# Kernel tuning notes

Hardware: AMD Instinct MI355X
Metric: run time of the kernel (lower is better)

The kernel has to match this reference:

```python
import jax, jax.numpy as jnp
import numpy as np
from jax import lax

B, T, V, E, H = 64, 20, 32000, 256, 512
EPS = 1e-5


def _conv_bn_relu(x, w, b, g, beta, m, v):
    # x: (B,C,H,W), w: (O,I,3,3), stride 2, pad 1; BN in eval mode with running stats
    y = lax.conv_general_dilated(x, w, (2, 2), ((1, 1), (1, 1)),
                                 dimension_numbers=('NCHW', 'OIHW', 'NCHW'))
    y = y + b[None, :, None, None]
    inv = g / jnp.sqrt(v + EPS)
    y = y * inv[None, :, None, None] + (beta - m * inv)[None, :, None, None]
    return jax.nn.relu(y)


def setup_inputs() -> dict:
    key = jax.random.key(0)
    ks = iter(jax.random.split(key, 40))
    s = 0.05
    d = {}
    d['images'] = jax.random.normal(next(ks), (B, 3, 64, 64), jnp.float32)
    d['captions'] = jax.random.randint(next(ks), (B, T), 0, V)
    chans = [3, 64, 128, 256, 512]
    for i in range(4):
        ci, co = chans[i], chans[i + 1]
        d[f'conv{i+1}_w'] = jax.random.normal(next(ks), (co, ci, 3, 3), jnp.float32) * s
        d[f'conv{i+1}_b'] = jnp.zeros((co,), jnp.float32)
        d[f'bn{i+1}_g'] = jnp.ones((co,), jnp.float32)
        d[f'bn{i+1}_b'] = jnp.zeros((co,), jnp.float32)
        d[f'bn{i+1}_m'] = jnp.zeros((co,), jnp.float32)
        d[f'bn{i+1}_v'] = jnp.ones((co,), jnp.float32)
    d['proj_w'] = jax.random.normal(next(ks), (E, 512), jnp.float32) * s
    d['proj_b'] = jnp.zeros((E,), jnp.float32)
    d['emb'] = jax.random.normal(next(ks), (V, E), jnp.float32) * s
    d['att_wv'] = jax.random.normal(next(ks), (H, E), jnp.float32) * s
    d['att_bv'] = jnp.zeros((H,), jnp.float32)
    d['att_wt'] = jax.random.normal(next(ks), (H, H), jnp.float32) * s
    d['att_bt'] = jnp.zeros((H,), jnp.float32)
    d['att_wa'] = jax.random.normal(next(ks), (1, H), jnp.float32) * s
    d['att_ba'] = jnp.zeros((1,), jnp.float32)
    d['w_ih'] = jax.random.normal(next(ks), (4 * H, 2 * E), jnp.float32) * s
    d['w_hh'] = jax.random.normal(next(ks), (4 * H, H), jnp.float32) * s
    d['b_ih'] = jnp.zeros((4 * H,), jnp.float32)
    d['b_hh'] = jnp.zeros((4 * H,), jnp.float32)
    d['out_w'] = jax.random.normal(next(ks), (V, H), jnp.float32) * s
    d['out_b'] = jnp.zeros((V,), jnp.float32)
    return d


def reference(images, captions,
              conv1_w, conv1_b, bn1_g, bn1_b, bn1_m, bn1_v,
              conv2_w, conv2_b, bn2_g, bn2_b, bn2_m, bn2_v,
              conv3_w, conv3_b, bn3_g, bn3_b, bn3_m, bn3_v,
              conv4_w, conv4_b, bn4_g, bn4_b, bn4_m, bn4_v,
              proj_w, proj_b, emb,
              att_wv, att_bv, att_wt, att_bt, att_wa, att_ba,
              w_ih, w_hh, b_ih, b_hh, out_w, out_b):
    # --- image encoder ---
    x = _conv_bn_relu(images, conv1_w, conv1_b, bn1_g, bn1_b, bn1_m, bn1_v)
    x = _conv_bn_relu(x, conv2_w, conv2_b, bn2_g, bn2_b, bn2_m, bn2_v)
    x = _conv_bn_relu(x, conv3_w, conv3_b, bn3_g, bn3_b, bn3_m, bn3_v)
    x = _conv_bn_relu(x, conv4_w, conv4_b, bn4_g, bn4_b, bn4_m, bn4_v)  # (B,512,4,4)
    b, c, h_, w_ = x.shape
    visual = x.reshape(b, c, h_ * w_).transpose(0, 2, 1)  # (B,R=16,512)
    visual = visual @ proj_w.T + proj_b                    # (B,R,E)

    v_proj = visual @ att_wv.T + att_bv                    # (B,R,H) - precompute

    emb_seq = emb[captions].transpose(1, 0, 2)             # (T,B,E)

    def step(carry, word_embed):
        h, cst = carry
        # attention over regions conditioned on previous h
        t = h @ att_wt.T + att_bt                          # (B,H)
        comb = jnp.tanh(v_proj + t[:, None, :])            # (B,R,H)
        scores = jnp.einsum('brh,h->br', comb, att_wa[0]) + att_ba[0]
        attw = jax.nn.softmax(scores, axis=1)              # (B,R)
        attended = jnp.einsum('br,bre->be', attw, visual)  # (B,E)
        xin = jnp.concatenate([word_embed, attended], axis=1)  # (B,2E)
        gates = xin @ w_ih.T + b_ih + h @ w_hh.T + b_hh    # (B,4H)
        i, f, g, o = jnp.split(gates, 4, axis=1)           # torch gate order i,f,g,o
        cst = jax.nn.sigmoid(f) * cst + jax.nn.sigmoid(i) * jnp.tanh(g)
        h = jax.nn.sigmoid(o) * jnp.tanh(cst)
        logits = h @ out_w.T + out_b                       # (B,V)
        return (h, cst), logits

    h0 = jnp.zeros((b, H), visual.dtype)
    c0 = jnp.zeros((b, H), visual.dtype)
    _, logits = lax.scan(step, (h0, c0), emb_seq)          # (T,B,V)
    return logits.transpose(1, 0, 2)                       # (B,T,V)
```

## Files before the change

kernel.cpp:

```cpp
#include <hip/hip_runtime.h>
#include <hip/hip_bf16.h>
#include <cstdint>
#include <cstddef>

typedef __attribute__((ext_vector_type(8))) short short8;
typedef __attribute__((ext_vector_type(4))) float floatx4;

__device__ inline float bf2f(unsigned short u) {
  union { unsigned int i; float f; } v; v.i = ((unsigned int)u) << 16; return v.f;
}
__device__ inline unsigned short f2bf(float f) {
  union { float f; unsigned int i; } v; v.f = f;
  unsigned int u = v.i;
  return (unsigned short)((u + 0x7FFFu + ((u >> 16) & 1u)) >> 16);
}
__device__ inline short8 ld8(const unsigned short* p) {
  return *reinterpret_cast<const short8*>(p);
}
__device__ inline float sigmoidf_(float x) { return 1.0f / (1.0f + __expf(-x)); }
__device__ inline float tanh_fast(float x) {
  float e = __expf(2.0f * x);
  return 1.0f - 2.0f / (e + 1.0f);
}

#define AT_LD(p)    __hip_atomic_load((p), __ATOMIC_RELAXED, __HIP_MEMORY_SCOPE_AGENT)
#define AT_ST(p, v) __hip_atomic_store((p), (v), __ATOMIC_RELAXED, __HIP_MEMORY_SCOPE_AGENT)
#define WAITCNT0()  asm volatile("s_waitcnt vmcnt(0) lgkmcnt(0)" ::: "memory")
#define CFENCE()    asm volatile("" ::: "memory")

static const size_t OFF_WIH   = 0;
static const size_t OFF_WHH   = 2097152;
static const size_t OFF_VPROJ = 4194304;
static const size_t OFF_VISE  = 5242880;
static const size_t OFF_HS    = 5767168;
static const size_t OFF_XIN   = 7077888;
static const size_t OFF_H0    = 7143424;
static const size_t OFF_H1    = 7208960;
static const size_t OFF_CT    = 7274496;
static const size_t OFF_W1PAD = 7405568;
static const size_t OFF_CW2   = 7409664;
static const size_t OFF_CW3   = 7557120;
static const size_t OFF_CW4   = 8146944;
static const size_t OFF_PRJW  = 10506240;
static const size_t OFF_ATWV  = 10768384;
static const size_t OFF_ACT1  = 11030528;
static const size_t OFF_ACT3  = 11030528;
static const size_t OFF_ACT2  = 19419136;
static const size_t OFF_ACT4  = 19419136;
static const size_t OFF_VISA  = 20467712;
static const size_t OFF_COL   = 23613440;
static const size_t OFF_BAR   = 28332032;
static const size_t OFF_ATWT  = 28348416;
static const size_t OFF_BIG   = 28872704;
static const size_t NEED_BIG  = OFF_BIG + 32768000;

__global__ void cvt_k(const float* __restrict__ s, unsigned short* __restrict__ d, int n4)
{
  int i = blockIdx.x * 256 + threadIdx.x;
  if (i < n4) {
    float4 v = reinterpret_cast<const float4*>(s)[i];
    ushort4 o;
    o.x = f2bf(v.x); o.y = f2bf(v.y); o.z = f2bf(v.z); o.w = f2bf(v.w);
    reinterpret_cast<ushort4*>(d)[i] = o;
  }
}

struct CvtArgs {
  const float* s[8];
  unsigned short* d[8];
  int cum[9];
};
__global__ void cvtall_k(CvtArgs a)
{
  int i = blockIdx.x * 256 + threadIdx.x;
  if (i >= a.cum[8]) return;
  int seg = 0;
  while (seg < 7 && i >= a.cum[seg + 1]) ++seg;
  int j = i - a.cum[seg];
  float4 v = reinterpret_cast<const float4*>(a.s[seg])[j];
  ushort4 o;
  o.x = f2bf(v.x); o.y = f2bf(v.y); o.z = f2bf(v.z); o.w = f2bf(v.w);
  reinterpret_cast<ushort4*>(a.d[seg])[j] = o;
}

__global__ void init_k(const float* __restrict__ conv1_w, unsigned short* __restrict__ w1pad,
                       unsigned short* __restrict__ h0, unsigned int* __restrict__ bar)
{
  int i = blockIdx.x * 256 + threadIdx.x;
  if (i < 64 * 32) {
    int co = i >> 5, k = i & 31;
    w1pad[i] = (k < 27) ? f2bf(conv1_w[co * 27 + k]) : (unsigned short)0;
  }
  if (i < 64 * 512) h0[i] = 0;
  if (i < 4096) bar[i] = 0u;
}

__global__ void im2col1_k(const float* __restrict__ in, unsigned short* __restrict__ col)
{
  int o = blockIdx.x * 256 + threadIdx.x;
  int n = o >> 5, k = o & 31;
  unsigned short v = 0;
  if (k < 27) {
    int b = n >> 10, y = (n >> 5) & 31, x = n & 31;
    int ci = k / 9, r9 = k - ci * 9, ky = r9 / 3, kx = r9 - ky * 3;
    int iy = 2 * y - 1 + ky, ix = 2 * x - 1 + kx;
    if (iy >= 0 && iy < 64 && ix >= 0 && ix < 64)
      v = f2bf(in[(((size_t)b * 3 + ci) << 12) + (iy << 6) + ix]);
  }
  col[o] = v;
}

__global__ void im2col_k(const unsigned short* __restrict__ in, unsigned short* __restrict__ col,
                         int Cin, int Hin, int Win, int Kreal, int Kpad, int lgHW, int lgW,
                         int n0)
{
  const int ng = n0 + blockIdx.x;
  const int b = ng >> lgHW;
  const int yx = ng & ((1 << lgHW) - 1);
  const int y = yx >> lgW;
  const int x = yx & ((1 << lgW) - 1);
  const int iy0 = 2 * y - 1;
  const int ix0 = 2 * x - 1;
  for (int k = threadIdx.x; k < Kpad; k += blockDim.x) {
    unsigned short v = 0;
    if (k < Kreal) {
      int ci = k / 9;
      int r9 = k - ci * 9;
      int ky = r9 / 3;
      int kx = r9 - ky * 3;
      int iy = iy0 + ky, ix = ix0 + kx;
      if (iy >= 0 && iy < Hin && ix >= 0 && ix < Win) {
        size_t idx = (((size_t)b * Cin + ci) * Hin + iy) * Win + ix;
        v = in[idx];
      }
    }
    col[(size_t)blockIdx.x * Kpad + k] = v;
  }
}

__global__ void visa_k(const unsigned short* __restrict__ act4, unsigned short* __restrict__ visA)
{
  int o = blockIdx.x * 256 + threadIdx.x;
  int c = o & 511, br = o >> 9;
  int b = br >> 4, r = br & 15;
  visA[o] = act4[(((size_t)b * 512 + c) << 4) + r];
}

template<int EPI>
__global__ __launch_bounds__(256)
void gemm_k(const unsigned short* __restrict__ A, const unsigned short* __restrict__ B,
            int K, int N, void* __restrict__ outp,
            const float* __restrict__ cb, const float* __restrict__ bg,
            const float* __restrict__ bb, const float* __restrict__ bm,
            const float* __restrict__ bv, int Cout, int lgHW,
            const float* __restrict__ biasN, int n_base, int ldOut)
{
  const int w   = threadIdx.x >> 6;
  const int l   = threadIdx.x & 63;
  const int l15 = l & 15;
  const int q   = l >> 4;
  const int m0  = blockIdx.y * 64;
  const int n0  = blockIdx.x * 256 + w * 64;
  const unsigned short* Ap = A + (size_t)(m0 + l15) * K + q * 8;
  const unsigned short* Bp = B + (size_t)(n0 + l15) * K + q * 8;

  floatx4 acc[4][4];
  #pragma unroll
  for (int i = 0; i < 4; i++)
    #pragma unroll
    for (int j = 0; j < 4; j++)
      acc[i][j] = (floatx4){0.f, 0.f, 0.f, 0.f};

  for (int kc = 0; kc < K; kc += 32) {
    short8 a0 = ld8(Ap + kc);
    short8 a1 = ld8(Ap + (size_t)16 * K + kc);
    short8 a2 = ld8(Ap + (size_t)32 * K + kc);
    short8 a3 = ld8(Ap + (size_t)48 * K + kc);
    #pragma unroll
    for (int nf = 0; nf < 4; nf++) {
      short8 bf = ld8(Bp + (size_t)(nf * 16) * K + kc);
      acc[0][nf] = __builtin_amdgcn_mfma_f32_16x16x32_bf16(a0, bf, acc[0][nf], 0, 0, 0);
      acc[1][nf] = __builtin_amdgcn_mfma_f32_16x16x32_bf16(a1, bf, acc[1][nf], 0, 0, 0);
      acc[2][nf] = __builtin_amdgcn_mfma_f32_16x16x32_bf16(a2, bf, acc[2][nf], 0, 0, 0);
      acc[3][nf] = __builtin_amdgcn_mfma_f32_16x16x32_bf16(a3, bf, acc[3][nf], 0, 0, 0);
    }
  }
  #pragma unroll
  for (int mf = 0; mf < 4; mf++) {
    #pragma unroll
    for (int r = 0; r < 4; r++) {
      int m = m0 + mf * 16 + q * 4 + r;
      float scale = 1.0f, shift = 0.0f;
      if (EPI == 0) {
        float inv = bg[m] / sqrtf(bv[m] + 1e-5f);
        scale = inv;
        shift = (cb[m] - bm[m]) * inv + bb[m];
      }
      #pragma unroll
      for (int nf = 0; nf < 4; nf++) {
        int n = n0 + nf * 16 + l15;
        float c = acc[mf][nf][r];
        if (EPI == 0) {
          c = fmaxf(c * scale + shift, 0.0f);
          int ng = n_base + n;
          int bi = ng >> lgHW;
          int yx = ng & ((1 << lgHW) - 1);
          ((unsigned short*)outp)[(((size_t)bi * Cout + m) << lgHW) + yx] = f2bf(c);
        } else if (EPI == 1) {
          ((unsigned short*)outp)[(size_t)m * N + n] = f2bf(c + biasN[n]);
        } else {
          ((float*)outp)[(size_t)m * ldOut + n_base + n] = c + biasN[n_base + n];
        }
      }
    }
  }
}

__global__ __launch_bounds__(256)
void rec_k(const unsigned short* __restrict__ w_ih, const unsigned short* __restrict__ w_hh,
           const float* __restrict__ b_ih, const float* __restrict__ b_hh,
           const unsigned short* __restrict__ vproj, const unsigned short* __restrict__ visE,
           const unsigned short* __restrict__ atwt, const float* __restrict__ att_bt,
           const float* __restrict__ att_wa, const float* __restrict__ att_ba,
           const int* __restrict__ captions, const float* __restrict__ emb,
           unsigned int* xin_u, unsigned int* h0_u, unsigned int* h1_u,
           unsigned short* __restrict__ hs, unsigned int* __restrict__ bar)
{
  __shared__ __align__(16) float sH[512];
  __shared__ float sT[512];
  __shared__ float sA[256];
  __shared__ float sSc[16];
  __shared__ float sAw[16];
  __shared__ __align__(16) unsigned short sB[64 * 256];
  __shared__ float sG[4][16][64];

  unsigned int* xf = bar;
  unsigned int* hf = bar + 64;

  const int tid = threadIdx.x;
  const int bid = blockIdx.x;
  const int w   = tid >> 6;
  const int l   = tid & 63;
  const int l15 = l & 15;
  const int q   = l >> 4;
  const int u0  = bid * 16;
  const int arow = w * 512 + u0 + l15;
  const unsigned short* wihRow = w_ih + (size_t)arow * 512;
  const unsigned short* whhRow = w_hh + (size_t)arow * 512;

  float creg[4];
  float bsum[4][4];
  if (bid < 32) {
    const int batch = tid & 63;
    const int g0 = tid >> 6;
    (void)batch;
    #pragma unroll
    for (int s = 0; s < 4; ++s) {
      creg[s] = 0.0f;
      int u = u0 + g0 * 4 + s;
      #pragma unroll
      for (int g = 0; g < 4; ++g)
        bsum[s][g] = b_ih[g * 512 + u] + b_hh[g * 512 + u];
    }
  }

  #define STAGE_TILE(SRC_EXPR)                                              \
    {                                                                       \
      _Pragma("unroll")                                                     \
      for (int i_ = 0; i_ < 16; ++i_) {                                     \
        int p_ = i_ * 256 + tid;                                            \
        int row_ = p_ >> 6, cu_ = p_ & 63;                                  \
        unsigned long long v_ = (SRC_EXPR);                                 \
        reinterpret_cast<unsigned long long*>(sB)[(row_ * 64 + cu_) ^ ((row_ & 7) << 1)] = v_; \
      }                                                                     \
    }

  #define MFMA_SEG(APTR)                                                    \
    {                                                                       \
      const unsigned short* Ap_ = (APTR);                                   \
      _Pragma("unroll")                                                     \
      for (int kc = 0; kc < 256; kc += 32) {                                \
        short8 a_ = ld8(Ap_ + kc);                                          \
        _Pragma("unroll")                                                   \
        for (int nt = 0; nt < 4; ++nt) {                                    \
          int row_ = l15 + nt * 16;                                         \
          short8 bf_ = *reinterpret_cast<const short8*>(                    \
              sB + ((row_ * 256 + q * 8 + kc) ^ ((row_ & 7) << 3)));        \
          acc[nt] = __builtin_amdgcn_mfma_f32_16x16x32_bf16(a_, bf_, acc[nt], 0, 0, 0); \
        }                                                                   \
      }                                                                     \
    }

  for (int t = 0; t < 20; ++t) {
    unsigned int* hin_u  = (t & 1) ? h1_u : h0_u;
    unsigned int* hout_u = (t & 1) ? h0_u : h1_u;

    if (t > 0) {
      if (tid < 32) {
        while ((int)AT_LD(hf + tid) < t) __builtin_amdgcn_s_sleep(1);
      }
      __syncthreads();
      CFENCE();
    }

    {
      const int b = bid;
      unsigned int hv = AT_LD(hin_u + b * 256 + tid);
      sH[2 * tid]     = bf2f((unsigned short)(hv & 0xffffu));
      sH[2 * tid + 1] = bf2f((unsigned short)(hv >> 16));
      __syncthreads();

      {
        const unsigned short* w0 = atwt + (size_t)tid * 512;
        const unsigned short* w1 = w0 + (size_t)256 * 512;
        float a0 = 0.f, a1 = 0.f;
        #pragma unroll 2
        for (int k = 0; k < 512; k += 8) {
          short8 x0 = ld8(w0 + k);
          short8 x1 = ld8(w1 + k);
          #pragma unroll
          for (int j = 0; j < 8; ++j) {
            float hk = sH[k + j];
            a0 += bf2f((unsigned short)x0[j]) * hk;
            a1 += bf2f((unsigned short)x1[j]) * hk;
          }
        }
        sT[tid]       = a0 + att_bt[tid];
        sT[tid + 256] = a1 + att_bt[tid + 256];
      }
      __syncthreads();

      {
        int r = tid >> 4, l16 = tid & 15;
        const unsigned short* vp = vproj + ((size_t)b * 16 + r) * 512;
        float s = 0.0f;
        #pragma unroll 4
        for (int i = 0; i < 32; ++i) {
          int k = i * 16 + l16;
          s += tanh_fast(bf2f(vp[k]) + sT[k]) * att_wa[k];
        }
        for (int d = 8; d >= 1; d >>= 1) s += __shfl_down(s, d, 16);
        if (l16 == 0) sSc[r] = s + att_ba[0];
      }
      __syncthreads();

      if (tid < 16) {
        float s = sSc[tid];
        float m = s;
        for (int d = 8; d >= 1; d >>= 1) m = fmaxf(m, __shfl_xor(m, d, 16));
        float e = __expf(s - m);
        float sum = e;
        for (int d = 8; d >= 1; d >>= 1) sum += __shfl_xor(sum, d, 16);
        sAw[tid] = e / sum;
      }
      __syncthreads();

      {
        float a = 0.0f;
        #pragma unroll
        for (int r = 0; r < 16; r++)
          a += sAw[r] * bf2f(visE[((size_t)b * 16 + r) * 256 + tid]);
        sA[tid] = a;
      }
      __syncthreads();

      if (tid < 128) {
        AT_ST(xin_u + b * 128 + tid,
              (unsigned int)f2bf(sA[2 * tid]) | ((unsigned int)f2bf(sA[2 * tid + 1]) << 16));
      }
      WAITCNT0();
      __syncthreads();
      if (tid == 0) AT_ST(xf + bid, (unsigned int)(t + 1));
    }

    if (bid < 32) {
      floatx4 acc[4];
      #pragma unroll
      for (int nt = 0; nt < 4; nt++) acc[nt] = (floatx4){0.f, 0.f, 0.f, 0.f};

      {
        #pragma unroll
        for (int i_ = 0; i_ < 16; ++i_) {
          int p_ = i_ * 256 + tid;
          int row_ = p_ >> 6, c4_ = p_ & 63;
          int cap_ = captions[row_ * 20 + t];
          float4 ev = *reinterpret_cast<const float4*>(emb + (size_t)cap_ * 256 + c4_ * 4);
          unsigned long long v_ =
              (unsigned long long)f2bf(ev.x) |
              ((unsigned long long)f2bf(ev.y) << 16) |
              ((unsigned long long)f2bf(ev.z) << 32) |
              ((unsigned long long)f2bf(ev.w) << 48);
          reinterpret_cast<unsigned long long*>(sB)[(row_ * 64 + c4_) ^ ((row_ & 7) << 1)] = v_;
        }
      }
      __syncthreads();
      MFMA_SEG(wihRow + q * 8);
      __syncthreads();

      const unsigned long long* hull = reinterpret_cast<const unsigned long long*>(hin_u);
      STAGE_TILE(AT_LD(hull + ((i_ * 256 + tid) >> 6) * 128 + ((i_ * 256 + tid) & 63)));
      __syncthreads();
      MFMA_SEG(whhRow + q * 8);
      __syncthreads();
      STAGE_TILE(AT_LD(hull + ((i_ * 256 + tid) >> 6) * 128 + 64 + ((i_ * 256 + tid) & 63)));
      __syncthreads();
      MFMA_SEG(whhRow + 256 + q * 8);
      __syncthreads();

      if (tid < 64) {
        while ((int)AT_LD(xf + tid) < t + 1) __builtin_amdgcn_s_sleep(1);
      }
      __syncthreads();
      CFENCE();

      const unsigned long long* xull = reinterpret_cast<const unsigned long long*>(xin_u);
      STAGE_TILE(AT_LD(xull + ((i_ * 256 + tid) >> 6) * 64 + ((i_ * 256 + tid) & 63)));
      __syncthreads();
      MFMA_SEG(wihRow + 256 + q * 8);
      __syncthreads();

      #pragma unroll
      for (int nt = 0; nt < 4; nt++)
        #pragma unroll
        for (int r = 0; r < 4; r++)
          sG[w][q * 4 + r][nt * 16 + l15] = acc[nt][r];
      __syncthreads();

      const int batch = tid & 63;
      const int g0 = tid >> 6;
      #pragma unroll
      for (int s = 0; s < 4; s += 2) {
        float hn2[2];
        #pragma unroll
        for (int d = 0; d < 2; ++d) {
          int um = g0 * 4 + s + d;
          float ii = sG[0][um][batch] + bsum[s + d][0];
          float ff = sG[1][um][batch] + bsum[s + d][1];
          float gg = sG[2][um][batch] + bsum[s + d][2];
          float oo = sG[3][um][batch] + bsum[s + d][3];
          float cn = sigmoidf_(ff) * creg[s + d] + sigmoidf_(ii) * tanh_fast(gg);
          hn2[d] = sigmoidf_(oo) * tanh_fast(cn);
          creg[s + d] = cn;
        }
        int u = u0 + g0 * 4 + s;
        unsigned int hp = (unsigned int)f2bf(hn2[0]) | ((unsigned int)f2bf(hn2[1]) << 16);
        AT_ST(hout_u + batch * 256 + (u >> 1), hp);
        *reinterpret_cast<unsigned int*>(hs + ((size_t)batch * 20 + t) * 512 + u) = hp;
      }
      WAITCNT0();
      __syncthreads();
      if (tid == 0) AT_ST(hf + bid, (unsigned int)(t + 1));
    }
  }
  #undef STAGE_TILE
  #undef MFMA_SEG
}

extern "C" void kernel_launch(void* const* d_in, const int* in_sizes, int n_in,
                              void* d_out, int out_size, void* d_ws, size_t ws_size,
                              hipStream_t stream)
{
  const float* images   = (const float*)d_in[0];
  const int*   captions = (const int*)d_in[1];
  const float* cw[4] = {(const float*)d_in[2],  (const float*)d_in[8],
                        (const float*)d_in[14], (const float*)d_in[20]};
  const float* cbp[4] = {(const float*)d_in[3],  (const float*)d_in[9],
                         (const float*)d_in[15], (const float*)d_in[21]};
  const float* bgp[4] = {(const float*)d_in[4],  (const float*)d_in[10],
                         (const float*)d_in[16], (const float*)d_in[22]};
  const float* bbp[4] = {(const float*)d_in[5],  (const float*)d_in[11],
                         (const float*)d_in[17], (const float*)d_in[23]};
  const float* bmp[4] = {(const float*)d_in[6],  (const float*)d_in[12],
                         (const float*)d_in[18], (const float*)d_in[24]};
  const float* bvp[4] = {(const float*)d_in[7],  (const float*)d_in[13],
                         (const float*)d_in[19], (const float*)d_in[25]};
  const float* proj_w = (const float*)d_in[26];
  const float* proj_b = (const float*)d_in[27];
  const float* emb    = (const float*)d_in[28];
  const float* att_wv = (const float*)d_in[29];
  const float* att_bv = (const float*)d_in[30];
  const float* att_wt = (const float*)d_in[31];
  const float* att_bt = (const float*)d_in[32];
  const float* att_wa = (const float*)d_in[33];
  const float* att_ba = (const float*)d_in[34];
  const float* w_ih   = (const float*)d_in[35];
  const float* w_hh   = (const float*)d_in[36];
  const float* b_ih   = (const float*)d_in[37];
  const float* b_hh   = (const float*)d_in[38];
  const float* out_w  = (const float*)d_in[39];
  const float* out_b  = (const float*)d_in[40];

  char* W = (char*)d_ws;
  unsigned short* wih_b = (unsigned short*)(W + OFF_WIH);
  unsigned short* whh_b = (unsigned short*)(W + OFF_WHH);
  unsigned short* vproj = (unsigned short*)(W + OFF_VPROJ);
  unsigned short* visE  = (unsigned short*)(W + OFF_VISE);
  unsigned short* hs    = (unsigned short*)(W + OFF_HS);
  unsigned short* xin   = (unsigned short*)(W + OFF_XIN);
  unsigned short* h0    = (unsigned short*)(W + OFF_H0);
  unsigned short* h1    = (unsigned short*)(W + OFF_H1);
  unsigned short* w1pad = (unsigned short*)(W + OFF_W1PAD);
  unsigned short* cw2_b = (unsigned short*)(W + OFF_CW2);
  unsigned short* cw3_b = (unsigned short*)(W + OFF_CW3);
  unsigned short* cw4_b = (unsigned short*)(W + OFF_CW4);
  unsigned short* prw_b = (unsigned short*)(W + OFF_PRJW);
  unsigned short* awv_b = (unsigned short*)(W + OFF_ATWV);
  unsigned short* atwt_b= (unsigned short*)(W + OFF_ATWT);
  unsigned short* act1  = (unsigned short*)(W + OFF_ACT1);
  unsigned short* act2  = (unsigned short*)(W + OFF_ACT2);
  unsigned short* act3  = (unsigned short*)(W + OFF_ACT3);
  unsigned short* act4  = (unsigned short*)(W + OFF_ACT4);
  unsigned short* visA  = (unsigned short*)(W + OFF_VISA);
  unsigned short* col   = (unsigned short*)(W + OFF_COL);
  unsigned int*   bar   = (unsigned int*)(W + OFF_BAR);
  const bool big = (ws_size >= NEED_BIG);
  unsigned short* colb  = big ? (unsigned short*)(W + OFF_BIG) : col;

  init_k<<<128, 256, 0, stream>>>(cw[0], w1pad, h0, bar);

  {
    CvtArgs ca;
    ca.s[0] = w_ih;   ca.d[0] = wih_b;
    ca.s[1] = w_hh;   ca.d[1] = whh_b;
    ca.s[2] = cw[1];  ca.d[2] = cw2_b;
    ca.s[3] = cw[2];  ca.d[3] = cw3_b;
    ca.s[4] = cw[3];  ca.d[4] = cw4_b;
    ca.s[5] = proj_w; ca.d[5] = prw_b;
    ca.s[6] = att_wv; ca.d[6] = awv_b;
    ca.s[7] = att_wt; ca.d[7] = atwt_b;
    int c0 = 0;
    int cnt[8] = {262144, 262144, 18432, 73728, 294912, 32768, 32768, 65536};
    ca.cum[0] = 0;
    for (int i = 0; i < 8; i++) { c0 += cnt[i]; ca.cum[i + 1] = c0; }
    cvtall_k<<<(c0 + 255) / 256, 256, 0, stream>>>(ca);
  }

  im2col1_k<<<8192, 256, 0, stream>>>(images, col);
  gemm_k<0><<<dim3(256, 1), 256, 0, stream>>>(w1pad, col, 32, 65536, act1,
      cbp[0], bgp[0], bbp[0], bmp[0], bvp[0], 64, 10, nullptr, 0, 0);

  if (big) {
    im2col_k<<<16384, 256, 0, stream>>>(act1, colb, 64, 32, 32, 576, 576, 8, 4, 0);
    gemm_k<0><<<dim3(64, 2), 256, 0, stream>>>(cw2_b, colb, 576, 16384, act2,
        cbp[1], bgp[1], bbp[1], bmp[1], bvp[1], 128, 8, nullptr, 0, 0);
    im2col_k<<<4096, 256, 0, stream>>>(act2, colb, 128, 16, 16, 1152, 1152, 6, 3, 0);
    gemm_k<0><<<dim3(16, 4), 256, 0, stream>>>(cw3_b, colb, 1152, 4096, act3,
        cbp[2], bgp[2], bbp[2], bmp[2], bvp[2], 256, 6, nullptr, 0, 0);
  } else {
    for (int c = 0; c < 4; c++) {
      im2col_k<<<4096, 256, 0, stream>>>(act1, col, 64, 32, 32, 576, 576, 8, 4, c * 4096);
      gemm_k<0><<<dim3(16, 2), 256, 0, stream>>>(cw2_b, col, 576, 4096, act2,
          cbp[1], bgp[1], bbp[1], bmp[1], bvp[1], 128, 8, nullptr, c * 4096, 0);
    }
    for (int c = 0; c < 2; c++) {
      im2col_k<<<2048, 256, 0, stream>>>(act2, col, 128, 16, 16, 1152, 1152, 6, 3, c * 2048);
      gemm_k<0><<<dim3(8, 4), 256, 0, stream>>>(cw3_b, col, 1152, 2048, act3,
          cbp[2], bgp[2], bbp[2], bmp[2], bvp[2], 256, 6, nullptr, c * 2048, 0);
    }
  }
  im2col_k<<<1024, 256, 0, stream>>>(act3, col, 256, 8, 8, 2304, 2304, 4, 2, 0);
  gemm_k<0><<<dim3(4, 8), 256, 0, stream>>>(cw4_b, col, 2304, 1024, act4,
      cbp[3], bgp[3], bbp[3], bmp[3], bvp[3], 512, 4, nullptr, 0, 0);

  visa_k<<<2048, 256, 0, stream>>>(act4, visA);
  gemm_k<1><<<dim3(1, 16), 256, 0, stream>>>(visA, prw_b, 512, 256, visE,
      nullptr, nullptr, nullptr, nullptr, nullptr, 0, 0, proj_b, 0, 0);
  gemm_k<1><<<dim3(2, 16), 256, 0, stream>>>(visE, awv_b, 256, 512, vproj,
      nullptr, nullptr, nullptr, nullptr, nullptr, 0, 0, att_bv, 0, 0);

  rec_k<<<64, 256, 0, stream>>>(wih_b, whh_b, b_ih, b_hh, vproj, visE,
                                atwt_b, att_bt, att_wa, att_ba, captions, emb,
                                (unsigned int*)xin, (unsigned int*)h0, (unsigned int*)h1,
                                hs, bar);

  if (big) {
    unsigned short* owb = (unsigned short*)(W + OFF_BIG);
    cvt_k<<<16000, 256, 0, stream>>>(out_w, owb, 32000 * 512 / 4);
    gemm_k<2><<<dim3(125, 20), 256, 0, stream>>>(hs, owb, 512, 32000,
        d_out, nullptr, nullptr, nullptr, nullptr, nullptr, 0, 0, out_b, 0, 32000);
  } else {
    for (int c = 0; c < 8; c++) {
      int rows = (c < 7) ? 4096 : 3328;
      const float* src = out_w + (size_t)c * 4096 * 512;
      cvt_k<<<rows / 2, 256, 0, stream>>>(src, col, rows * 512 / 4);
      gemm_k<2><<<dim3(rows / 256, 20), 256, 0, stream>>>(hs, col, 512, rows,
          d_out, nullptr, nullptr, nullptr, nullptr, nullptr, 0, 0, out_b, c * 4096, 32000);
    }
  }
}
```

Before: 1.687 ms.

## Use per-timestep buffers and flags in recurrent kernel, skip t=0 h work

The recurrent kernel now writes x and h into separate per-timestep buffers and signals completion with per-timestep boolean flags, replacing double-buffered h and monotonic counters. Reads of those buffers become plain loads instead of atomic loads. The t=0 attention matvec and W_hh MFMA are skipped because h0 is zero, and flag clearing moves into visa_k, so init_k no longer zeroes h0. This reduces per-step synchronization and load overhead in a latency-bound loop, at the cost of more workspace and a reliance on plain loads seeing data published before the flag.

Measured after the change: 1.551 ms. 1.09x faster.

```diff
diff --git a/kernel.cpp b/kernel.cpp
--- a/kernel.cpp
+++ b/kernel.cpp
@@ -33,10 +33,6 @@
 static const size_t OFF_VPROJ = 4194304;
 static const size_t OFF_VISE  = 5242880;
 static const size_t OFF_HS    = 5767168;
-static const size_t OFF_XIN   = 7077888;
-static const size_t OFF_H0    = 7143424;
-static const size_t OFF_H1    = 7208960;
-static const size_t OFF_CT    = 7274496;
 static const size_t OFF_W1PAD = 7405568;
 static const size_t OFF_CW2   = 7409664;
 static const size_t OFF_CW3   = 7557120;
@@ -48,8 +44,10 @@
 static const size_t OFF_ACT2  = 19419136;
 static const size_t OFF_ACT4  = 19419136;
 static const size_t OFF_VISA  = 20467712;
+static const size_t OFF_XB    = 21516288;
+static const size_t OFF_HB    = 22171648;
+static const size_t OFF_FLG   = 23482368;
 static const size_t OFF_COL   = 23613440;
-static const size_t OFF_BAR   = 28332032;
 static const size_t OFF_ATWT  = 28348416;
 static const size_t OFF_BIG   = 28872704;
 static const size_t NEED_BIG  = OFF_BIG + 32768000;
@@ -83,16 +81,13 @@
   reinterpret_cast<ushort4*>(a.d[seg])[j] = o;
 }
 
-__global__ void init_k(const float* __restrict__ conv1_w, unsigned short* __restrict__ w1pad,
-                       unsigned short* __restrict__ h0, unsigned int* __restrict__ bar)
+__global__ void init_k(const float* __restrict__ conv1_w, unsigned short* __restrict__ w1pad)
 {
   int i = blockIdx.x * 256 + threadIdx.x;
   if (i < 64 * 32) {
     int co = i >> 5, k = i & 31;
     w1pad[i] = (k < 27) ? f2bf(conv1_w[co * 27 + k]) : (unsigned short)0;
   }
-  if (i < 64 * 512) h0[i] = 0;
-  if (i < 4096) bar[i] = 0u;
 }
 
 __global__ void im2col1_k(const float* __restrict__ in, unsigned short* __restrict__ col)
@@ -138,12 +133,14 @@
   }
 }
 
-__global__ void visa_k(const unsigned short* __restrict__ act4, unsigned short* __restrict__ visA)
+__global__ void visa_k(const unsigned short* __restrict__ act4, unsigned short* __restrict__ visA,
+                       unsigned int* __restrict__ flg)
 {
   int o = blockIdx.x * 256 + threadIdx.x;
   int c = o & 511, br = o >> 9;
   int b = br >> 4, r = br & 15;
   visA[o] = act4[(((size_t)b * 512 + c) << 4) + r];
+  if (o < 2560) AT_ST(flg + o, 0u);
 }
 
 template<int EPI>
@@ -223,8 +220,8 @@
            const unsigned short* __restrict__ atwt, const float* __restrict__ att_bt,
            const float* __restrict__ att_wa, const float* __restrict__ att_ba,
            const int* __restrict__ captions, const float* __restrict__ emb,
-           unsigned int* xin_u, unsigned int* h0_u, unsigned int* h1_u,
-           unsigned short* __restrict__ hs, unsigned int* __restrict__ bar)
+           unsigned int* xb, unsigned int* hb, unsigned int* flg,
+           unsigned short* __restrict__ hs)
 {
   __shared__ __align__(16) float sH[512];
   __shared__ float sT[512];
@@ -233,9 +230,6 @@
   __shared__ float sAw[16];
   __shared__ __align__(16) unsigned short sB[64 * 256];
   __shared__ float sG[4][16][64];
-
-  unsigned int* xf = bar;
-  unsigned int* hf = bar + 64;
 
   const int tid = threadIdx.x;
   const int bid = blockIdx.x;
@@ -251,9 +245,7 @@
   float creg[4];
   float bsum[4][4];
   if (bid < 32) {
-    const int batch = tid & 63;
     const int g0 = tid >> 6;
-    (void)batch;
     #pragma unroll
     for (int s = 0; s < 4; ++s) {
       creg[s] = 0.0f;
@@ -292,12 +284,15 @@
     }
 
   for (int t = 0; t < 20; ++t) {
-    unsigned int* hin_u  = (t & 1) ? h1_u : h0_u;
-    unsigned int* hout_u = (t & 1) ? h0_u : h1_u;
+    const unsigned int* hbin = hb + (size_t)(t - 1) * 16384;
+    unsigned int* hbout = hb + (size_t)t * 16384;
+    unsigned int* xbt   = xb + (size_t)t * 8192;
+    unsigned int* flgt  = flg + (size_t)t * 128;
 
     if (t > 0) {
       if (tid < 32) {
-        while ((int)AT_LD(hf + tid) < t) __builtin_amdgcn_s_sleep(1);
+        while (AT_LD(flg + (size_t)(t - 1) * 128 + 64 + tid) == 0u)
+          __builtin_amdgcn_s_sleep(1);
       }
       __syncthreads();
       CFENCE();
@@ -305,12 +300,12 @@
 
     {
       const int b = bid;
-      unsigned int hv = AT_LD(hin_u + b * 256 + tid);
-      sH[2 * tid]     = bf2f((unsigned short)(hv & 0xffffu));
-      sH[2 * tid + 1] = bf2f((unsigned short)(hv >> 16));
-      __syncthreads();
-
-      {
+      if (t > 0) {
+        unsigned int hv = hbin[b * 256 + tid];
+        sH[2 * tid]     = bf2f((unsigned short)(hv & 0xffffu));
+        sH[2 * tid + 1] = bf2f((unsigned short)(hv >> 16));
+        __syncthreads();
+
         const unsigned short* w0 = atwt + (size_t)tid * 512;
         const unsigned short* w1 = w0 + (size_t)256 * 512;
         float a0 = 0.f, a1 = 0.f;
@@ -327,6 +322,9 @@
         }
         sT[tid]       = a0 + att_bt[tid];
         sT[tid + 256] = a1 + att_bt[tid + 256];
+      } else {
+        sT[tid]       = att_bt[tid];
+        sT[tid + 256] = att_bt[tid + 256];
       }
       __syncthreads();
 
@@ -364,13 +362,18 @@
       }
       __syncthreads();
 
-      if (tid < 128) {
-        AT_ST(xin_u + b * 128 + tid,
-              (unsigned int)f2bf(sA[2 * tid]) | ((unsigned int)f2bf(sA[2 * tid + 1]) << 16));
+      if (tid < 64) {
+        int j = 4 * tid;
+        unsigned long long v =
+            (unsigned long long)f2bf(sA[j]) |
+            ((unsigned long long)f2bf(sA[j + 1]) << 16) |
+            ((unsigned long long)f2bf(sA[j + 2]) << 32) |
+            ((unsigned long long)f2bf(sA[j + 3]) << 48);
+        AT_ST(reinterpret_cast<unsigned long long*>(xbt) + b * 64 + tid, v);
       }
       WAITCNT0();
       __syncthreads();
-      if (tid == 0) AT_ST(xf + bid, (unsigned int)(t + 1));
+      if (tid == 0) AT_ST(flgt + bid, 1u);
     }
 
     if (bid < 32) {
@@ -397,24 +400,26 @@
       MFMA_SEG(wihRow + q * 8);
       __syncthreads();
 
-      const unsigned long long* hull = reinterpret_cast<const unsigned long long*>(hin_u);
-      STAGE_TILE(AT_LD(hull + ((i_ * 256 + tid) >> 6) * 128 + ((i_ * 256 + tid) & 63)));
-      __syncthreads();
-      MFMA_SEG(whhRow + q * 8);
-      __syncthreads();
-      STAGE_TILE(AT_LD(hull + ((i_ * 256 + tid) >> 6) * 128 + 64 + ((i_ * 256 + tid) & 63)));
-      __syncthreads();
-      MFMA_SEG(whhRow + 256 + q * 8);
-      __syncthreads();
+      if (t > 0) {
+        const unsigned long long* hull = reinterpret_cast<const unsigned long long*>(hbin);
+        STAGE_TILE(hull[((i_ * 256 + tid) >> 6) * 128 + ((i_ * 256 + tid) & 63)]);
+        __syncthreads();
+        MFMA_SEG(whhRow + q * 8);
+        __syncthreads();
+        STAGE_TILE(hull[((i_ * 256 + tid) >> 6) * 128 + 64 + ((i_ * 256 + tid) & 63)]);
+        __syncthreads();
+        MFMA_SEG(whhRow + 256 + q * 8);
+        __syncthreads();
+      }
 
       if (tid < 64) {
-        while ((int)AT_LD(xf + tid) < t + 1) __builtin_amdgcn_s_sleep(1);
+        while (AT_LD(flgt + tid) == 0u) __builtin_amdgcn_s_sleep(1);
       }
       __syncthreads();
       CFENCE();
 
-      const unsigned long long* xull = reinterpret_cast<const unsigned long long*>(xin_u);
-      STAGE_TILE(AT_LD(xull + ((i_ * 256 + tid) >> 6) * 64 + ((i_ * 256 + tid) & 63)));
+      const unsigned long long* xull = reinterpret_cast<const unsigned long long*>(xbt);
+      STAGE_TILE(xull[((i_ * 256 + tid) >> 6) * 64 + ((i_ * 256 + tid) & 63)]);
       __syncthreads();
       MFMA_SEG(wihRow + 256 + q * 8);
       __syncthreads();
@@ -444,12 +449,12 @@
         }
         int u = u0 + g0 * 4 + s;
         unsigned int hp = (unsigned int)f2bf(hn2[0]) | ((unsigned int)f2bf(hn2[1]) << 16);
-        AT_ST(hout_u + batch * 256 + (u >> 1), hp);
+        AT_ST(hbout + batch * 256 + (u >> 1), hp);
         *reinterpret_cast<unsigned int*>(hs + ((size_t)batch * 20 + t) * 512 + u) = hp;
       }
       WAITCNT0();
       __syncthreads();
-      if (tid == 0) AT_ST(hf + bid, (unsigned int)(t + 1));
+      if (tid == 0) AT_ST(flgt + 64 + bid, 1u);
     }
   }
   #undef STAGE_TILE
@@ -496,9 +501,6 @@
   unsigned short* vproj = (unsigned short*)(W + OFF_VPROJ);
   unsigned short* visE  = (unsigned short*)(W + OFF_VISE);
   unsigned short* hs    = (unsigned short*)(W + OFF_HS);
-  unsigned short* xin   = (unsigned short*)(W + OFF_XIN);
-  unsigned short* h0    = (unsigned short*)(W + OFF_H0);
-  unsigned short* h1    = (unsigned short*)(W + OFF_H1);
   unsigned short* w1pad = (unsigned short*)(W + OFF_W1PAD);
   unsigned short* cw2_b = (unsigned short*)(W + OFF_CW2);
   unsigned short* cw3_b = (unsigned short*)(W + OFF_CW3);
@@ -512,11 +514,13 @@
   unsigned short* act4  = (unsigned short*)(W + OFF_ACT4);
   unsigned short* visA  = (unsigned short*)(W + OFF_VISA);
   unsigned short* col   = (unsigned short*)(W + OFF_COL);
-  unsigned int*   bar   = (unsigned int*)(W + OFF_BAR);
+  unsigned int*   xbp   = (unsigned int*)(W + OFF_XB);
+  unsigned int*   hbp   = (unsigned int*)(W + OFF_HB);
+  unsigned int*   flg   = (unsigned int*)(W + OFF_FLG);
   const bool big = (ws_size >= NEED_BIG);
   unsigned short* colb  = big ? (unsigned short*)(W + OFF_BIG) : col;
 
-  init_k<<<128, 256, 0, stream>>>(cw[0], w1pad, h0, bar);
+  init_k<<<8, 256, 0, stream>>>(cw[0], w1pad);
 
   {
     CvtArgs ca;
@@ -562,7 +566,7 @@
   gemm_k<0><<<dim3(4, 8), 256, 0, stream>>>(cw4_b, col, 2304, 1024, act4,
       cbp[3], bgp[3], bbp[3], bmp[3], bvp[3], 512, 4, nullptr, 0, 0);
 
-  visa_k<<<2048, 256, 0, stream>>>(act4, visA);
+  visa_k<<<2048, 256, 0, stream>>>(act4, visA, flg);
   gemm_k<1><<<dim3(1, 16), 256, 0, stream>>>(visA, prw_b, 512, 256, visE,
       nullptr, nullptr, nullptr, nullptr, nullptr, 0, 0, proj_b, 0, 0);
   gemm_k<1><<<dim3(2, 16), 256, 0, stream>>>(visE, awv_b, 256, 512, vproj,
@@ -570,8 +574,7 @@
 
   rec_k<<<64, 256, 0, stream>>>(wih_b, whh_b, b_ih, b_hh, vproj, visE,
                                 atwt_b, att_bt, att_wa, att_ba, captions, emb,
-                                (unsigned int*)xin, (unsigned int*)h0, (unsigned int*)h1,
-                                hs, bar);
+                                xbp, hbp, flg, hs);
 
   if (big) {
     unsigned short* owb = (unsigned short*)(W + OFF_BIG);
```
